# Performance work log

Measured on AMD Instinct MI355X. Metric: run time of the kernel, lower is better.

## Reference

```python
import jax, jax.numpy as jnp
import numpy as np

B, T, D = 4, 1024, 1024
H = 16
DH = D // H            # head dim (attention_dim/num_heads)
FF = 4096
EPS = 1e-6             # allennlp LayerNorm eps
NEG = jnp.finfo(jnp.float32).min


def _layer_norm(x, g, b):
    # allennlp LayerNorm: (x - mean) / (unbiased_std + eps) * gamma + beta
    mean = jnp.mean(x, axis=-1, keepdims=True)
    var = jnp.var(x, axis=-1, keepdims=True) * (x.shape[-1] / (x.shape[-1] - 1))
    return g * (x - mean) / (jnp.sqrt(var) + EPS) + b


def setup_inputs() -> dict:
    key = jax.random.key(0)
    ks = jax.random.split(key, 12)
    s = lambda fan_in: 1.0 / np.sqrt(fan_in)
    return {
        "src": jax.random.normal(ks[0], (B, T, D), jnp.float32),
        "src_mask": jnp.ones((B, T), jnp.int32),
        # weights stored [in, out]
        "q_w": jax.random.uniform(ks[1], (D, D), jnp.float32, -s(D), s(D)),
        "q_b": jnp.zeros((D,), jnp.float32),
        "kv_w": jax.random.uniform(ks[2], (D, 2 * D), jnp.float32, -s(D), s(D)),
        "kv_b": jnp.zeros((2 * D,), jnp.float32),
        "out_w": jax.random.uniform(ks[3], (D, D), jnp.float32, -s(D), s(D)),
        "out_b": jnp.zeros((D,), jnp.float32),
        "ffn_w1": jax.random.uniform(ks[4], (D, FF), jnp.float32, -s(D), s(D)),
        "ffn_b1": jnp.zeros((FF,), jnp.float32),
        "ffn_w2": jax.random.uniform(ks[5], (FF, D), jnp.float32, -s(FF), s(FF)),
        "ffn_b2": jnp.zeros((D,), jnp.float32),
        "norm1_g": jnp.ones((D,), jnp.float32),
        "norm1_b": jnp.zeros((D,), jnp.float32),
        "norm2_g": jnp.ones((D,), jnp.float32),
        "norm2_b": jnp.zeros((D,), jnp.float32),
    }


def reference(src, src_mask, q_w, q_b, kv_w, kv_b, out_w, out_b,
              ffn_w1, ffn_b1, ffn_w2, ffn_b2,
              norm1_g, norm1_b, norm2_g, norm2_b):
    b, t, d = src.shape
    scale = jnp.asarray(DH ** 0.5, src.dtype)

    q = (src @ q_w + q_b).reshape(b, t, H, DH)
    kv = src @ kv_w + kv_b                         # (b,t,2D): first half keys, second half values
    k = kv[..., :D].reshape(b, t, H, DH)
    v = kv[..., D:].reshape(b, t, H, DH)

    # scaled dot-product: queries divided by sqrt(head_dim) before bmm
    logits = jnp.einsum("bqhd,bkhd->bhqk", q / scale, k)
    # memory_efficient masked_softmax: masked key positions -> dtype min
    mask = src_mask[:, None, None, :].astype(bool)  # (b,1,1,t) over keys
    logits = jnp.where(mask, logits, NEG)
    attn = jax.nn.softmax(logits, axis=-1)          # dropout off (eval)

    ctx = jnp.einsum("bhqk,bkhd->bqhd", attn, v).reshape(b, t, D)
    attn_out = ctx @ out_w + out_b

    out1 = _layer_norm(src + attn_out, norm1_g, norm1_b)
    ffn = jax.nn.relu(out1 @ ffn_w1 + ffn_b1) @ ffn_w2 + ffn_b2
    out2 = _layer_norm(out1 + ffn, norm2_g, norm2_b)
    return out2
```

## Files before the change

### kernel.cpp

```cpp
#include <hip/hip_runtime.h>

#define DEV __device__ __forceinline__
#define SB0 __builtin_amdgcn_sched_barrier(0)

typedef unsigned short u16;
typedef __attribute__((ext_vector_type(4))) float f32x4;
typedef __attribute__((ext_vector_type(8))) short short8;

DEV u16 f2bf(float f) {
  union { float f; unsigned u; } c; c.f = f;
  unsigned u = c.u;
  unsigned r = (u + 0x7FFFu + ((u >> 16) & 1u)) >> 16;
  return (u16)r;
}
DEV float bf2f(u16 h) {
  union { unsigned u; float f; } c; c.u = ((unsigned)h) << 16;
  return c.f;
}
DEV unsigned cvtpk(float a, float b) {
  unsigned r;
  asm("v_cvt_pk_bf16_f32 %0, %1, %2" : "=v"(r) : "v"(a), "v"(b));
  return r;
}

DEV void gload16(const void* g, void* l) {
  __builtin_amdgcn_global_load_lds(
      (__attribute__((address_space(1))) void*)(g),
      (__attribute__((address_space(3))) void*)(l), 16, 0, 0);
}
template <int N> DEV void vmcw() {
  if constexpr (N == 0) asm volatile("s_waitcnt vmcnt(0)" ::: "memory");
  else if constexpr (N == 8) asm volatile("s_waitcnt vmcnt(8)" ::: "memory");
  SB0;
}

__global__ __launch_bounds__(256) void prep_kernel(
    const float* __restrict__ src, const float* __restrict__ q_w,
    const float* __restrict__ kv_w, const float* __restrict__ out_w,
    const float* __restrict__ w1, const float* __restrict__ w2,
    u16* __restrict__ Xbf, u16* __restrict__ WqkvT, u16* __restrict__ WoT,
    u16* __restrict__ W1T, u16* __restrict__ W2T) {
  __shared__ float tile[32 * 33];
  int bb = blockIdx.x, tid = threadIdx.x;
  if (bb < 4096) {
    int i = bb * 256 + tid;
    float4 v = reinterpret_cast<const float4*>(src)[i];
    ushort4 o;
    o.x = f2bf(v.x); o.y = f2bf(v.y); o.z = f2bf(v.z); o.w = f2bf(v.w);
    reinterpret_cast<ushort4*>(Xbf)[i] = o;
    return;
  }
  const float* in; u16* outp; int ld_in, ld_out, bx, by;
  if (bb < 5120)       { int t = bb - 4096;  in = q_w;   outp = WqkvT; ld_in = 1024; ld_out = 1024; bx = t & 31;  by = t >> 5; }
  else if (bb < 7168)  { int t = bb - 5120;  in = kv_w;  outp = WqkvT + (size_t)1024 * 1024; ld_in = 2048; ld_out = 1024; bx = t & 63;  by = t >> 6; }
  else if (bb < 8192)  { int t = bb - 7168;  in = out_w; outp = WoT;   ld_in = 1024; ld_out = 1024; bx = t & 31;  by = t >> 5; }
  else if (bb < 12288) { int t = bb - 8192;  in = w1;    outp = W1T;   ld_in = 4096; ld_out = 1024; bx = t & 127; by = t >> 7; }
  else                 { int t = bb - 12288; in = w2;    outp = W2T;   ld_in = 1024; ld_out = 4096; bx = t & 31;  by = t >> 5; }
  int tx = tid & 31, ty = tid >> 5;
  int c0 = bx * 32, r0 = by * 32;
#pragma unroll
  for (int j = 0; j < 4; ++j)
    tile[(ty + j * 8) * 33 + tx] = in[(size_t)(r0 + ty + j * 8) * ld_in + c0 + tx];
  __syncthreads();
#pragma unroll
  for (int j = 0; j < 4; ++j)
    outp[(size_t)(c0 + ty + j * 8) * ld_out + r0 + tx] = f2bf(tile[tx * 33 + ty + j * 8]);
}

__global__ __launch_bounds__(256) void transpose_vtp_kernel(
    const u16* __restrict__ in, u16* __restrict__ out) {
  __shared__ float tile[32][33];
  int c0 = blockIdx.x * 32, r0 = blockIdx.y * 32;
  int tx = threadIdx.x, ty = threadIdx.y;
#pragma unroll
  for (int j = 0; j < 4; ++j)
    tile[ty + j * 8][tx] = bf2f(in[(size_t)(r0 + ty + j * 8) * 3072 + 2048 + c0 + tx]);
  __syncthreads();
  int k = r0 + tx;
  int base = k & ~63, kb = k & 63;
  int n = kb >> 4, w = kb & 15;
  int p = ((n >> 1) << 5) | ((w >> 2) << 3) | ((n & 1) << 2) | (w & 3);
#pragma unroll
  for (int j = 0; j < 4; ++j)
    out[(size_t)(c0 + ty + j * 8) * 4096 + base + p] = f2bf(tile[tx][ty + j * 8]);
}

template <int BM, int BN, int WM, int WN, int RING, int OCC, typename OutT, bool RELU>
__global__ __launch_bounds__(WM * WN * 64, OCC) void gemm_ring_kernel(
    const u16* __restrict__ A, int lda,
    const u16* __restrict__ Bt, int ldb,
    const float* __restrict__ bias, const float* __restrict__ bias2, int split,
    OutT* __restrict__ C, int ldc, size_t c_off, int K, float scale) {
  constexpr int NWAVE = WM * WN;
  constexpr int MT = BM / WM / 16;
  constexpr int NF = BN / WN / 16;
  constexpr int LPT = (BM + BN) / 16 / NWAVE;
  constexpr int DEPTH = RING - 1;
  constexpr int SLOT = (BM + BN) * 32;
  static_assert(LPT == 4, "vmcnt constants assume LPT==4");
  __shared__ __align__(16) u16 ring[RING][SLOT];

  const int tid = threadIdx.x;
  const int lane = tid & 63, wid = tid >> 6;
  const int wr = wid / WN, wc = wid % WN;
  const int lr = lane & 15, hi = lane >> 4;
  const int z = blockIdx.z;

  const int gx = gridDim.x;
  const int nwg = gx * gridDim.y;
  const int orig = blockIdx.y * gx + blockIdx.x;
  const int q = nwg >> 3, r8 = nwg & 7, xcd = orig & 7, oo = orig >> 3;
  const int lid = (xcd < r8 ? xcd * (q + 1) : r8 * (q + 1) + (xcd - r8) * q) + oo;
  const int rb = lid / gx, cb = lid % gx;

  const u16* Abase = A + (size_t)rb * BM * lda + (size_t)z * K;
  const u16* Bbase = Bt + (size_t)cb * BN * ldb + (size_t)z * K;
  C += (size_t)z * c_off;

  auto stage = [&](int slot, int kt) {
#pragma unroll
    for (int j = 0; j < LPT; ++j) {
      int u = wid * LPT + j;
      int rloc = u * 16 + (lane >> 2);
      int cs = (lane & 3) ^ ((rloc >> 1) & 3);
      const u16* src;
      if (u < BM / 16) src = Abase + (size_t)rloc * lda + kt * 32 + cs * 8;
      else src = Bbase + (size_t)(rloc - BM) * ldb + kt * 32 + cs * 8;
      gload16(src, &ring[slot][u * 512]);
    }
  };

  f32x4 acc[MT][NF];
  const f32x4 zero = {0.f, 0.f, 0.f, 0.f};
#pragma unroll
  for (int m = 0; m < MT; ++m)
#pragma unroll
    for (int n = 0; n < NF; ++n) acc[m][n] = zero;

  const int NT = K >> 5;
  stage(0, 0); stage(1, 1); stage(2, 2);
  vmcw<8>();
  __builtin_amdgcn_s_barrier(); SB0;

  const int sw = (lr >> 1) & 3;
  int sl = 0, st = DEPTH;
  for (int k = 0; k < NT; ++k) {
    const u16* la = &ring[sl][0];
    const u16* lb = &ring[sl][BM * 32];
    short8 bf[NF], af[MT];
#pragma unroll
    for (int n = 0; n < NF; ++n)
      bf[n] = *(const short8*)(lb + (wc * (BN / WN) + n * 16 + lr) * 32 + ((hi ^ sw) * 8));
#pragma unroll
    for (int m = 0; m < MT; ++m)
      af[m] = *(const short8*)(la + (wr * (BM / WM) + m * 16 + lr) * 32 + ((hi ^ sw) * 8));
    if (k + DEPTH < NT) stage(st, k + DEPTH);
    __builtin_amdgcn_s_setprio(1);
#pragma unroll
    for (int m = 0; m < MT; ++m)
#pragma unroll
      for (int n = 0; n < NF; ++n)
        acc[m][n] = __builtin_amdgcn_mfma_f32_16x16x32_bf16(af[m], bf[n], acc[m][n], 0, 0, 0);
    __builtin_amdgcn_s_setprio(0);
    if (k + RING < NT) vmcw<8>();
    else if (k + 1 < NT) vmcw<0>();
    __builtin_amdgcn_s_barrier(); SB0;
    sl = (sl == RING - 1) ? 0 : sl + 1;
    st = (st == RING - 1) ? 0 : st + 1;
  }

#pragma unroll
  for (int m = 0; m < MT; ++m) {
    int row0 = rb * BM + wr * (BM / WM) + m * 16 + hi * 4;
#pragma unroll
    for (int n = 0; n < NF; ++n) {
      int col = cb * BN + wc * (BN / WN) + n * 16 + lr;
      float sc = (col < split) ? scale : 1.0f;
      float bv = 0.0f;
      if (z == 0) bv = (col < split) ? bias[col] : bias2[col - split];
#pragma unroll
      for (int r = 0; r < 4; ++r) {
        float v = (acc[m][n][r] + bv) * sc;
        if (RELU) v = fmaxf(v, 0.0f);
        if constexpr (sizeof(OutT) == 2)
          C[(size_t)(row0 + r) * ldc + col] = f2bf(v);
        else
          C[(size_t)(row0 + r) * ldc + col] = v;
      }
    }
  }
}

__global__ __launch_bounds__(512, 2) void attn_kernel(
    const u16* __restrict__ QKV, const u16* __restrict__ Vtp,
    const int* __restrict__ mask, u16* __restrict__ CTX) {
  __shared__ __align__(16) u16 kl[2][64 * 64];
  __shared__ __align__(16) u16 vl[2][64 * 64];
  __shared__ unsigned long long mask_lds[16];
  const int lane = threadIdx.x & 63;
  const int wid = threadIdx.x >> 6;
  const int lr = lane & 15, hi = lane >> 4;
  const int bh = blockIdx.x, qt = blockIdx.y;
  const int b = bh >> 4, h = bh & 15;

  const size_t qrow = (size_t)(b * 1024 + qt * 128 + wid * 16 + lr);
  short8 qf[2];
#pragma unroll
  for (int ks = 0; ks < 2; ++ks)
    qf[ks] = *(const short8*)(QKV + qrow * 3072 + h * 64 + ks * 32 + hi * 8);

#pragma unroll
  for (int i = 0; i < 2; ++i) {
    int kt = wid * 2 + i;
    unsigned long long bal = __ballot(mask[b * 1024 + kt * 64 + lane] != 0);
    if (lane == 0) mask_lds[kt] = bal;
  }

  const u16* Kbase = QKV + (size_t)(b * 1024) * 3072 + 1024 + h * 64;
  const u16* Vbase = Vtp + (size_t)(h * 64) * 4096 + b * 1024;

  auto stage = [&](int bf, int kt) {
    int r = wid * 8 + (lane >> 3);
    int cs = (lane & 7) ^ (r & 7);
    gload16(Kbase + (size_t)(kt * 64 + r) * 3072 + cs * 8, &kl[bf][wid * 8 * 64]);
    gload16(Vbase + (size_t)r * 4096 + kt * 64 + cs * 8, &vl[bf][wid * 8 * 64]);
  };

  float m_run = -3.0e38f, l_run = 0.0f;
  f32x4 O[4];
  const f32x4 zero = {0.f, 0.f, 0.f, 0.f};
#pragma unroll
  for (int d = 0; d < 4; ++d) O[d] = zero;

  stage(0, 0);
  __syncthreads();
  int cur = 0;
  for (int kt = 0; kt < 16; ++kt) {
    if (kt + 1 < 16) stage(cur ^ 1, kt + 1);

    f32x4 s[4];
#pragma unroll
    for (int n = 0; n < 4; ++n) s[n] = zero;
    __builtin_amdgcn_s_setprio(1);
#pragma unroll
    for (int n = 0; n < 4; ++n) {
      int key = n * 16 + lr;
#pragma unroll
      for (int ks = 0; ks < 2; ++ks) {
        int ch = (hi + 4 * ks) ^ (key & 7);
        short8 kf = *(const short8*)(kl[cur] + key * 64 + ch * 8);
        s[n] = __builtin_amdgcn_mfma_f32_16x16x32_bf16(kf, qf[ks], s[n], 0, 0, 0);
      }
    }
    __builtin_amdgcn_s_setprio(0);

    unsigned long long mk = mask_lds[kt];
    if (mk != ~0ull) {
#pragma unroll
      for (int n = 0; n < 4; ++n)
#pragma unroll
        for (int r = 0; r < 4; ++r)
          if (!((mk >> (n * 16 + hi * 4 + r)) & 1ull)) s[n][r] = -3.0e38f;
    }

    float tm = -3.0e38f;
#pragma unroll
    for (int n = 0; n < 4; ++n)
      tm = fmaxf(tm, fmaxf(fmaxf(s[n][0], s[n][1]), fmaxf(s[n][2], s[n][3])));
    tm = fmaxf(tm, __shfl_xor(tm, 16));
    tm = fmaxf(tm, __shfl_xor(tm, 32));

    float mo = m_run;
    bool grow = __any(tm > mo);
    float mn = grow ? fmaxf(mo, tm) : mo;
    m_run = mn;
    float ps = 0.0f;
#pragma unroll
    for (int n = 0; n < 4; ++n)
#pragma unroll
      for (int r = 0; r < 4; ++r) {
        float p = __expf(s[n][r] - mn);
        s[n][r] = p;
        ps += p;
      }
    if (grow) {
      float alpha = __expf(mo - mn);
      l_run = l_run * alpha + ps;
#pragma unroll
      for (int d = 0; d < 4; ++d)
#pragma unroll
        for (int r = 0; r < 4; ++r) O[d][r] *= alpha;
    } else {
      l_run += ps;
    }

#pragma unroll
    for (int ks = 0; ks < 2; ++ks) {
      union { unsigned u[4]; short8 s8; } pf;
      pf.u[0] = cvtpk(s[2 * ks][0], s[2 * ks][1]);
      pf.u[1] = cvtpk(s[2 * ks][2], s[2 * ks][3]);
      pf.u[2] = cvtpk(s[2 * ks + 1][0], s[2 * ks + 1][1]);
      pf.u[3] = cvtpk(s[2 * ks + 1][2], s[2 * ks + 1][3]);
      __builtin_amdgcn_s_setprio(1);
#pragma unroll
      for (int d = 0; d < 4; ++d) {
        int vrow = d * 16 + lr;
        int ch = (hi + 4 * ks) ^ (vrow & 7);
        short8 vf = *(const short8*)(vl[cur] + vrow * 64 + ch * 8);
        O[d] = __builtin_amdgcn_mfma_f32_16x16x32_bf16(vf, pf.s8, O[d], 0, 0, 0);
      }
      __builtin_amdgcn_s_setprio(0);
    }
    __syncthreads();
    cur ^= 1;
  }

  float l = l_run;
  l += __shfl_xor(l, 16);
  l += __shfl_xor(l, 32);
  float inv = 1.0f / l;
#pragma unroll
  for (int dt = 0; dt < 4; ++dt) {
    uint2 w;
    w.x = cvtpk(O[dt][0] * inv, O[dt][1] * inv);
    w.y = cvtpk(O[dt][2] * inv, O[dt][3] * inv);
    *(uint2*)(CTX + qrow * 1024 + h * 64 + dt * 16 + hi * 4) = w;
  }
}

__global__ __launch_bounds__(256) void ln_kernel(
    const float* __restrict__ xa, const float* __restrict__ xb,
    const float* __restrict__ xc,
    const float* __restrict__ g, const float* __restrict__ beta,
    float* __restrict__ of, u16* __restrict__ ob) {
  int row = blockIdx.x;
  int tid = threadIdx.x;
  const float* pa = xa + (size_t)row * 1024;
  const float* pb = xb + (size_t)row * 1024;
  const float* pc = xc ? xc + (size_t)row * 1024 : nullptr;
  float v[4];
  float s = 0.f, s2 = 0.f;
#pragma unroll
  for (int j = 0; j < 4; ++j) {
    int c = tid + j * 256;
    float x = pa[c] + pb[c];
    if (pc) x += pc[c];
    v[j] = x; s += x; s2 += x * x;
  }
#pragma unroll
  for (int d = 1; d < 64; d <<= 1) {
    s += __shfl_xor(s, d);
    s2 += __shfl_xor(s2, d);
  }
  __shared__ float red[8];
  int w = tid >> 6, lane = tid & 63;
  if (lane == 0) { red[w] = s; red[4 + w] = s2; }
  __syncthreads();
  s = red[0] + red[1] + red[2] + red[3];
  s2 = red[4] + red[5] + red[6] + red[7];
  float mean = s * (1.0f / 1024.0f);
  float var = fmaxf((s2 - 1024.0f * mean * mean) * (1.0f / 1023.0f), 0.0f);
  float rden = 1.0f / (sqrtf(var) + 1e-6f);
#pragma unroll
  for (int j = 0; j < 4; ++j) {
    int c = tid + j * 256;
    float y = g[c] * (v[j] - mean) * rden + beta[c];
    of[(size_t)row * 1024 + c] = y;
    if (ob) ob[(size_t)row * 1024 + c] = f2bf(y);
  }
}

extern "C" void kernel_launch(void* const* d_in, const int* in_sizes, int n_in,
                              void* d_out, int out_size, void* d_ws, size_t ws_size,
                              hipStream_t stream) {
  const float* src   = (const float*)d_in[0];
  const int*   mask  = (const int*)d_in[1];
  const float* q_w   = (const float*)d_in[2];
  const float* q_b   = (const float*)d_in[3];
  const float* kv_w  = (const float*)d_in[4];
  const float* kv_b  = (const float*)d_in[5];
  const float* out_w = (const float*)d_in[6];
  const float* out_b = (const float*)d_in[7];
  const float* w1    = (const float*)d_in[8];
  const float* b1    = (const float*)d_in[9];
  const float* w2    = (const float*)d_in[10];
  const float* b2    = (const float*)d_in[11];
  const float* g1    = (const float*)d_in[12];
  const float* be1   = (const float*)d_in[13];
  const float* g2    = (const float*)d_in[14];
  const float* be2   = (const float*)d_in[15];
  float* out = (float*)d_out;

  char* ws = (char*)d_ws;
  const size_t MB = 1024 * 1024;
  const int BIG = 1 << 30;
  u16*  Xbf   = (u16*)(ws + 0);
  u16*  CTX   = (u16*)(ws + 8 * MB);
  u16*  WqkvT = (u16*)(ws + 16 * MB);
  u16*  WoT   = (u16*)(ws + 22 * MB);
  u16*  W1T   = (u16*)(ws + 24 * MB);
  u16*  W2T   = (u16*)(ws + 32 * MB);
  u16*  QKV   = (u16*)(ws + 40 * MB);
  u16*  Vtp   = (u16*)(ws + 64 * MB);
  u16*  F1b   = (u16*)(ws + 40 * MB);
  float* AOUT = (float*)(ws + 72 * MB);
  float* FP0  = (float*)(ws + 72 * MB);
  float* FP1  = (float*)(ws + 88 * MB);
  float* OUT1F= (float*)(ws + 104 * MB);
  u16*  OUT1B = (u16*)(ws + 0);

  prep_kernel<<<dim3(16384), dim3(256), 0, stream>>>(
      src, q_w, kv_w, out_w, w1, w2, Xbf, WqkvT, WoT, W1T, W2T);
  gemm_ring_kernel<256, 256, 2, 4, 4, 2, u16, false><<<dim3(12, 16), dim3(512), 0, stream>>>(
      Xbf, 1024, WqkvT, 1024, q_b, kv_b, 1024, QKV, 3072, 0, 1024, 0.125f);
  transpose_vtp_kernel<<<dim3(32, 128), dim3(32, 8), 0, stream>>>(QKV, Vtp);
  attn_kernel<<<dim3(64, 8), dim3(512), 0, stream>>>(QKV, Vtp, mask, CTX);
  gemm_ring_kernel<128, 128, 2, 2, 4, 2, float, false><<<dim3(8, 32), dim3(256), 0, stream>>>(
      CTX, 1024, WoT, 1024, out_b, nullptr, BIG, AOUT, 1024, 0, 1024, 1.0f);
  ln_kernel<<<dim3(4096), dim3(256), 0, stream>>>(src, AOUT, nullptr, g1, be1, OUT1F, OUT1B);
  gemm_ring_kernel<256, 256, 2, 4, 4, 2, u16, true><<<dim3(16, 16), dim3(512), 0, stream>>>(
      OUT1B, 1024, W1T, 1024, b1, nullptr, BIG, F1b, 4096, 0, 1024, 1.0f);
  gemm_ring_kernel<128, 128, 2, 2, 4, 2, float, false><<<dim3(8, 32, 2), dim3(256), 0, stream>>>(
      F1b, 4096, W2T, 4096, b2, nullptr, BIG, FP0, 1024,
      (size_t)(FP1 - FP0), 2048, 1.0f);
  ln_kernel<<<dim3(4096), dim3(256), 0, stream>>>(OUT1F, FP0, FP1, g2, be2, out, nullptr);
  (void)in_sizes; (void)n_in; (void)out_size; (void)ws_size;
}
```

Measured before the change: 325.6 us.

## Add four-phase interleaved 256x256 GEMM and split-K=4 FFN2 with bf16 partials

Adds a 256x256 GEMM variant that breaks each K-step into four phases. Each phase interleaves LDS fragment reads, one global->LDS stage load and 8 MFMAs, with barriers between phases, so memory traffic overlaps with compute more evenly. This kernel now handles the QKV and FFN1 GEMMs. FFN2 moves from 128x128 tiles with split-K=2 and fp32 partials to 256x256 tiles with split-K=4 writing bf16 partials. A new LN kernel sums the four bf16 partials plus the residual using vectorized loads, which cuts partial-sum traffic but adds bf16 rounding error on the FFN output before the residual add.

```diff
diff --git a/kernel.cpp b/kernel.cpp
--- a/kernel.cpp
+++ b/kernel.cpp
@@ -33,6 +33,7 @@
   else if constexpr (N == 8) asm volatile("s_waitcnt vmcnt(8)" ::: "memory");
   SB0;
 }
+DEV void lgkm0() { asm volatile("s_waitcnt lgkmcnt(0)" ::: "memory"); SB0; }
 
 __global__ __launch_bounds__(256) void prep_kernel(
     const float* __restrict__ src, const float* __restrict__ q_w,
@@ -85,57 +86,163 @@
     out[(size_t)(c0 + ty + j * 8) * 4096 + base + p] = f2bf(tile[tx][ty + j * 8]);
 }
 
-template <int BM, int BN, int WM, int WN, int RING, int OCC, typename OutT, bool RELU>
-__global__ __launch_bounds__(WM * WN * 64, OCC) void gemm_ring_kernel(
+template <typename OutT, bool RELU>
+__global__ __launch_bounds__(512, 2) void gemm_4ph_kernel(
     const u16* __restrict__ A, int lda,
     const u16* __restrict__ Bt, int ldb,
     const float* __restrict__ bias, const float* __restrict__ bias2, int split,
     OutT* __restrict__ C, int ldc, size_t c_off, int K, float scale) {
-  constexpr int NWAVE = WM * WN;
-  constexpr int MT = BM / WM / 16;
-  constexpr int NF = BN / WN / 16;
-  constexpr int LPT = (BM + BN) / 16 / NWAVE;
-  constexpr int DEPTH = RING - 1;
-  constexpr int SLOT = (BM + BN) * 32;
-  static_assert(LPT == 4, "vmcnt constants assume LPT==4");
+  constexpr int BM = 256, RING = 4, DEPTH = 3;
+  constexpr int SLOT = 512 * 32;
   __shared__ __align__(16) u16 ring[RING][SLOT];
 
   const int tid = threadIdx.x;
   const int lane = tid & 63, wid = tid >> 6;
-  const int wr = wid / WN, wc = wid % WN;
+  const int wr = wid >> 2, wc = wid & 3;
   const int lr = lane & 15, hi = lane >> 4;
   const int z = blockIdx.z;
 
   const int gx = gridDim.x;
   const int nwg = gx * gridDim.y;
   const int orig = blockIdx.y * gx + blockIdx.x;
-  const int q = nwg >> 3, r8 = nwg & 7, xcd = orig & 7, oo = orig >> 3;
-  const int lid = (xcd < r8 ? xcd * (q + 1) : r8 * (q + 1) + (xcd - r8) * q) + oo;
+  const int q8 = nwg >> 3, r8 = nwg & 7, xcd = orig & 7, oo = orig >> 3;
+  const int lid = (xcd < r8 ? xcd * (q8 + 1) : r8 * (q8 + 1) + (xcd - r8) * q8) + oo;
   const int rb = lid / gx, cb = lid % gx;
 
   const u16* Abase = A + (size_t)rb * BM * lda + (size_t)z * K;
-  const u16* Bbase = Bt + (size_t)cb * BN * ldb + (size_t)z * K;
+  const u16* Bbase = Bt + (size_t)cb * BM * ldb + (size_t)z * K;
   C += (size_t)z * c_off;
 
+  auto stage1 = [&](int slot, int kt, int j) {
+    int u = wid * 4 + j;
+    int rloc = u * 16 + (lane >> 2);
+    int cs = (lane & 3) ^ ((rloc >> 1) & 3);
+    const u16* src;
+    if (u < 16) src = Abase + (size_t)rloc * lda + kt * 32 + cs * 8;
+    else src = Bbase + (size_t)(rloc - BM) * ldb + kt * 32 + cs * 8;
+    gload16(src, &ring[slot][u * 512]);
+  };
+
+  f32x4 acc[8][4];
+  const f32x4 zero = {0.f, 0.f, 0.f, 0.f};
+#pragma unroll
+  for (int m = 0; m < 8; ++m)
+#pragma unroll
+    for (int n = 0; n < 4; ++n) acc[m][n] = zero;
+
+  const int NT = K >> 5;
+#pragma unroll
+  for (int s = 0; s < 3; ++s)
+#pragma unroll
+    for (int j = 0; j < 4; ++j) stage1(s, s, j);
+  vmcw<8>();
+  __builtin_amdgcn_s_barrier(); SB0;
+
+  const int co = ((hi ^ ((lr >> 1) & 3)) * 8);
+  int sl = 0, st = DEPTH;
+  for (int k = 0; k < NT; ++k) {
+    const u16* la = &ring[sl][0];
+    const u16* lb = &ring[sl][BM * 32];
+    const bool do_stage = (k + DEPTH) < NT;
+    short8 bf[4];
+#pragma unroll
+    for (int q = 0; q < 4; ++q) {
+      short8 af0 = *(const short8*)(la + (wr * 128 + (2 * q) * 16 + lr) * 32 + co);
+      short8 af1 = *(const short8*)(la + (wr * 128 + (2 * q + 1) * 16 + lr) * 32 + co);
+      if (q == 0) {
+#pragma unroll
+        for (int n = 0; n < 4; ++n)
+          bf[n] = *(const short8*)(lb + (wc * 64 + n * 16 + lr) * 32 + co);
+      }
+      if (do_stage) stage1(st, k + DEPTH, q);
+      __builtin_amdgcn_s_barrier(); SB0;
+      lgkm0();
+      __builtin_amdgcn_s_setprio(1);
+#pragma unroll
+      for (int n = 0; n < 4; ++n)
+        acc[2 * q][n] = __builtin_amdgcn_mfma_f32_16x16x32_bf16(af0, bf[n], acc[2 * q][n], 0, 0, 0);
+#pragma unroll
+      for (int n = 0; n < 4; ++n)
+        acc[2 * q + 1][n] = __builtin_amdgcn_mfma_f32_16x16x32_bf16(af1, bf[n], acc[2 * q + 1][n], 0, 0, 0);
+      __builtin_amdgcn_s_setprio(0);
+      if (q == 3) {
+        if (k + RING < NT) vmcw<8>();
+        else if (k + 1 < NT) vmcw<0>();
+      }
+      __builtin_amdgcn_s_barrier(); SB0;
+    }
+    sl = (sl + 1) & 3;
+    st = (st + 1) & 3;
+  }
+
+#pragma unroll
+  for (int m = 0; m < 8; ++m) {
+    int row0 = rb * BM + wr * 128 + m * 16 + hi * 4;
+#pragma unroll
+    for (int n = 0; n < 4; ++n) {
+      int col = cb * BM + wc * 64 + n * 16 + lr;
+      float sc = (col < split) ? scale : 1.0f;
+      float bv = 0.0f;
+      if (z == 0) bv = (col < split) ? bias[col] : bias2[col - split];
+#pragma unroll
+      for (int r = 0; r < 4; ++r) {
+        float v = (acc[m][n][r] + bv) * sc;
+        if (RELU) v = fmaxf(v, 0.0f);
+        if constexpr (sizeof(OutT) == 2)
+          C[(size_t)(row0 + r) * ldc + col] = f2bf(v);
+        else
+          C[(size_t)(row0 + r) * ldc + col] = v;
+      }
+    }
+  }
+}
+
+template <typename OutT, bool RELU>
+__global__ __launch_bounds__(256, 2) void gemm_ring_kernel(
+    const u16* __restrict__ A, int lda,
+    const u16* __restrict__ Bt, int ldb,
+    const float* __restrict__ bias, const float* __restrict__ bias2, int split,
+    OutT* __restrict__ C, int ldc, size_t c_off, int K, float scale) {
+  constexpr int BM = 128, RING = 4, DEPTH = 3;
+  constexpr int SLOT = 256 * 32;
+  __shared__ __align__(16) u16 ring[RING][SLOT];
+
+  const int tid = threadIdx.x;
+  const int lane = tid & 63, wid = tid >> 6;
+  const int wr = wid >> 1, wc = wid & 1;
+  const int lr = lane & 15, hi = lane >> 4;
+  const int z = blockIdx.z;
+
+  const int gx = gridDim.x;
+  const int nwg = gx * gridDim.y;
+  const int orig = blockIdx.y * gx + blockIdx.x;
+  const int q8 = nwg >> 3, r8 = nwg & 7, xcd = orig & 7, oo = orig >> 3;
+  const int lid = (xcd < r8 ? xcd * (q8 + 1) : r8 * (q8 + 1) + (xcd - r8) * q8) + oo;
+  const int rb = lid / gx, cb = lid % gx;
+
+  const u16* Abase = A + (size_t)rb * BM * lda + (size_t)z * K;
+  const u16* Bbase = Bt + (size_t)cb * BM * ldb + (size_t)z * K;
+  C += (size_t)z * c_off;
+
   auto stage = [&](int slot, int kt) {
 #pragma unroll
-    for (int j = 0; j < LPT; ++j) {
-      int u = wid * LPT + j;
+    for (int j = 0; j < 4; ++j) {
+      int u = wid * 4 + j;
       int rloc = u * 16 + (lane >> 2);
       int cs = (lane & 3) ^ ((rloc >> 1) & 3);
       const u16* src;
-      if (u < BM / 16) src = Abase + (size_t)rloc * lda + kt * 32 + cs * 8;
+      if (u < 8) src = Abase + (size_t)rloc * lda + kt * 32 + cs * 8;
       else src = Bbase + (size_t)(rloc - BM) * ldb + kt * 32 + cs * 8;
       gload16(src, &ring[slot][u * 512]);
     }
   };
 
-  f32x4 acc[MT][NF];
+  f32x4 acc[4][4];
   const f32x4 zero = {0.f, 0.f, 0.f, 0.f};
 #pragma unroll
-  for (int m = 0; m < MT; ++m)
-#pragma unroll
-    for (int n = 0; n < NF; ++n) acc[m][n] = zero;
+  for (int m = 0; m < 4; ++m)
+#pragma unroll
+    for (int n = 0; n < 4; ++n) acc[m][n] = zero;
 
   const int NT = K >> 5;
   stage(0, 0); stage(1, 1); stage(2, 2);
@@ -147,34 +254,34 @@
   for (int k = 0; k < NT; ++k) {
     const u16* la = &ring[sl][0];
     const u16* lb = &ring[sl][BM * 32];
-    short8 bf[NF], af[MT];
-#pragma unroll
-    for (int n = 0; n < NF; ++n)
-      bf[n] = *(const short8*)(lb + (wc * (BN / WN) + n * 16 + lr) * 32 + ((hi ^ sw) * 8));
-#pragma unroll
-    for (int m = 0; m < MT; ++m)
-      af[m] = *(const short8*)(la + (wr * (BM / WM) + m * 16 + lr) * 32 + ((hi ^ sw) * 8));
+    short8 bf[4], af[4];
+#pragma unroll
+    for (int n = 0; n < 4; ++n)
+      bf[n] = *(const short8*)(lb + (wc * 64 + n * 16 + lr) * 32 + ((hi ^ sw) * 8));
+#pragma unroll
+    for (int m = 0; m < 4; ++m)
+      af[m] = *(const short8*)(la + (wr * 64 + m * 16 + lr) * 32 + ((hi ^ sw) * 8));
     if (k + DEPTH < NT) stage(st, k + DEPTH);
     __builtin_amdgcn_s_setprio(1);
 #pragma unroll
-    for (int m = 0; m < MT; ++m)
-#pragma unroll
-      for (int n = 0; n < NF; ++n)
+    for (int m = 0; m < 4; ++m)
+#pragma unroll
+      for (int n = 0; n < 4; ++n)
         acc[m][n] = __builtin_amdgcn_mfma_f32_16x16x32_bf16(af[m], bf[n], acc[m][n], 0, 0, 0);
     __builtin_amdgcn_s_setprio(0);
     if (k + RING < NT) vmcw<8>();
     else if (k + 1 < NT) vmcw<0>();
     __builtin_amdgcn_s_barrier(); SB0;
-    sl = (sl == RING - 1) ? 0 : sl + 1;
-    st = (st == RING - 1) ? 0 : st + 1;
-  }
-
-#pragma unroll
-  for (int m = 0; m < MT; ++m) {
-    int row0 = rb * BM + wr * (BM / WM) + m * 16 + hi * 4;
-#pragma unroll
-    for (int n = 0; n < NF; ++n) {
-      int col = cb * BN + wc * (BN / WN) + n * 16 + lr;
+    sl = (sl + 1) & 3;
+    st = (st + 1) & 3;
+  }
+
+#pragma unroll
+  for (int m = 0; m < 4; ++m) {
+    int row0 = rb * BM + wr * 64 + m * 16 + hi * 4;
+#pragma unroll
+    for (int n = 0; n < 4; ++n) {
+      int col = cb * BM + wc * 64 + n * 16 + lr;
       float sc = (col < split) ? scale : 1.0f;
       float bv = 0.0f;
       if (z == 0) bv = (col < split) ? bias[col] : bias2[col - split];
@@ -330,21 +437,18 @@
 
 __global__ __launch_bounds__(256) void ln_kernel(
     const float* __restrict__ xa, const float* __restrict__ xb,
-    const float* __restrict__ xc,
     const float* __restrict__ g, const float* __restrict__ beta,
     float* __restrict__ of, u16* __restrict__ ob) {
   int row = blockIdx.x;
   int tid = threadIdx.x;
   const float* pa = xa + (size_t)row * 1024;
   const float* pb = xb + (size_t)row * 1024;
-  const float* pc = xc ? xc + (size_t)row * 1024 : nullptr;
   float v[4];
   float s = 0.f, s2 = 0.f;
 #pragma unroll
   for (int j = 0; j < 4; ++j) {
     int c = tid + j * 256;
     float x = pa[c] + pb[c];
-    if (pc) x += pc[c];
     v[j] = x; s += x; s2 += x * x;
   }
 #pragma unroll
@@ -368,6 +472,45 @@
     of[(size_t)row * 1024 + c] = y;
     if (ob) ob[(size_t)row * 1024 + c] = f2bf(y);
   }
+}
+
+__global__ __launch_bounds__(256) void ln2p_kernel(
+    const float* __restrict__ x1, const u16* __restrict__ p, size_t pstride,
+    const float* __restrict__ g, const float* __restrict__ beta,
+    float* __restrict__ out) {
+  int row = blockIdx.x;
+  int tid = threadIdx.x;
+  int c0 = tid * 4;
+  float4 v4 = *reinterpret_cast<const float4*>(x1 + (size_t)row * 1024 + c0);
+  float v[4] = {v4.x, v4.y, v4.z, v4.w};
+#pragma unroll
+  for (int i = 0; i < 4; ++i) {
+    ushort4 u4 = *reinterpret_cast<const ushort4*>(p + i * pstride + (size_t)row * 1024 + c0);
+    v[0] += bf2f(u4.x); v[1] += bf2f(u4.y); v[2] += bf2f(u4.z); v[3] += bf2f(u4.w);
+  }
+  float s = 0.f, s2 = 0.f;
+#pragma unroll
+  for (int j = 0; j < 4; ++j) { s += v[j]; s2 += v[j] * v[j]; }
+#pragma unroll
+  for (int d = 1; d < 64; d <<= 1) {
+    s += __shfl_xor(s, d);
+    s2 += __shfl_xor(s2, d);
+  }
+  __shared__ float red[8];
+  int w = tid >> 6, lane = tid & 63;
+  if (lane == 0) { red[w] = s; red[4 + w] = s2; }
+  __syncthreads();
+  s = red[0] + red[1] + red[2] + red[3];
+  s2 = red[4] + red[5] + red[6] + red[7];
+  float mean = s * (1.0f / 1024.0f);
+  float var = fmaxf((s2 - 1024.0f * mean * mean) * (1.0f / 1023.0f), 0.0f);
+  float rden = 1.0f / (sqrtf(var) + 1e-6f);
+  float4 o;
+  o.x = g[c0 + 0] * (v[0] - mean) * rden + beta[c0 + 0];
+  o.y = g[c0 + 1] * (v[1] - mean) * rden + beta[c0 + 1];
+  o.z = g[c0 + 2] * (v[2] - mean) * rden + beta[c0 + 2];
+  o.w = g[c0 + 3] * (v[3] - mean) * rden + beta[c0 + 3];
+  *reinterpret_cast<float4*>(out + (size_t)row * 1024 + c0) = o;
 }
 
 extern "C" void kernel_launch(void* const* d_in, const int* in_sizes, int n_in,
@@ -404,25 +547,25 @@
   u16*  Vtp   = (u16*)(ws + 64 * MB);
   u16*  F1b   = (u16*)(ws + 40 * MB);
   float* AOUT = (float*)(ws + 72 * MB);
-  float* FP0  = (float*)(ws + 72 * MB);
-  float* FP1  = (float*)(ws + 88 * MB);
-  float* OUT1F= (float*)(ws + 104 * MB);
-  u16*  OUT1B = (u16*)(ws + 0);
+  float* OUT1F= (float*)(ws + 88 * MB);
+  u16*  OUT1B = (u16*)(ws + 104 * MB);
+  u16*  FP    = (u16*)(ws + 0);
 
   prep_kernel<<<dim3(16384), dim3(256), 0, stream>>>(
       src, q_w, kv_w, out_w, w1, w2, Xbf, WqkvT, WoT, W1T, W2T);
-  gemm_ring_kernel<256, 256, 2, 4, 4, 2, u16, false><<<dim3(12, 16), dim3(512), 0, stream>>>(
+  gemm_4ph_kernel<u16, false><<<dim3(12, 16), dim3(512), 0, stream>>>(
       Xbf, 1024, WqkvT, 1024, q_b, kv_b, 1024, QKV, 3072, 0, 1024, 0.125f);
   transpose_vtp_kernel<<<dim3(32, 128), dim3(32, 8), 0, stream>>>(QKV, Vtp);
   attn_kernel<<<dim3(64, 8), dim3(512), 0, stream>>>(QKV, Vtp, mask, CTX);
-  gemm_ring_kernel<128, 128, 2, 2, 4, 2, float, false><<<dim3(8, 32), dim3(256), 0, stream>>>(
+  gemm_ring_kernel<float, false><<<dim3(8, 32), dim3(256), 0, stream>>>(
       CTX, 1024, WoT, 1024, out_b, nullptr, BIG, AOUT, 1024, 0, 1024, 1.0f);
-  ln_kernel<<<dim3(4096), dim3(256), 0, stream>>>(src, AOUT, nullptr, g1, be1, OUT1F, OUT1B);
-  gemm_ring_kernel<256, 256, 2, 4, 4, 2, u16, true><<<dim3(16, 16), dim3(512), 0, stream>>>(
+  ln_kernel<<<dim3(4096), dim3(256), 0, stream>>>(src, AOUT, g1, be1, OUT1F, OUT1B);
+  gemm_4ph_kernel<u16, true><<<dim3(16, 16), dim3(512), 0, stream>>>(
       OUT1B, 1024, W1T, 1024, b1, nullptr, BIG, F1b, 4096, 0, 1024, 1.0f);
-  gemm_ring_kernel<128, 128, 2, 2, 4, 2, float, false><<<dim3(8, 32, 2), dim3(256), 0, stream>>>(
-      F1b, 4096, W2T, 4096, b2, nullptr, BIG, FP0, 1024,
-      (size_t)(FP1 - FP0), 2048, 1.0f);
-  ln_kernel<<<dim3(4096), dim3(256), 0, stream>>>(OUT1F, FP0, FP1, g2, be2, out, nullptr);
+  gemm_4ph_kernel<u16, false><<<dim3(4, 16, 4), dim3(512), 0, stream>>>(
+      F1b, 4096, W2T, 4096, b2, nullptr, BIG, FP, 1024,
+      (size_t)(4 * MB), 1024, 1.0f);
+  ln2p_kernel<<<dim3(4096), dim3(256), 0, stream>>>(
+      OUT1F, FP, 4 * MB, g2, be2, out);
   (void)in_sizes; (void)n_in; (void)out_size; (void)ws_size;
 }
```

New measurement: 331.2 us. Within noise of the previous version (+1.7%).
